# Kernel optimization log

Hardware: AMD Instinct MI355X
Metric: run time of the kernel (lower is better)

## Reference

```python
import jax, jax.numpy as jnp
import numpy as np

SIZE = 128
WIN = SIZE // 4   # sliding-window size == region size (32)
HALF = WIN // 2   # 16


def _conv(x, w, pad, groups=1):
    return jax.lax.conv_general_dilated(x, w, (1, 1), [(pad, pad), (pad, pad)],
        dimension_numbers=('NCHW', 'OIHW', 'NCHW'), feature_group_count=groups)


def _resize(x, h, w):
    # F.interpolate(..., mode='bilinear', align_corners=False)
    return jax.image.resize(x, (x.shape[0], x.shape[1], h, w), 'bilinear', antialias=False)


def _gauss_kernels():
    ax = np.linspace(-2.0, 2.0, 5)
    xx, yy = np.meshgrid(ax, ax)
    g = np.exp(-(xx ** 2 + yy ** 2) / 2.0) / (2.0 * np.pi)  # sigma = 1
    gx = (-xx * g).astype(np.float32)
    gy = (-yy * g).astype(np.float32)
    return (jnp.asarray(np.tile(gx[None, None], (3, 3, 1, 1))),
            jnp.asarray(np.tile(gy[None, None], (3, 3, 1, 1))))


def _edge_extract(x):
    Gx, Gy = _gauss_kernels()
    h = _conv(x, Gx, 2)
    v = _conv(x, Gy, 2)
    return jnp.tanh(jnp.sqrt(h * h + v * v + 1e-8))


def _color_moments(x, win=5):
    # F.unfold-based local mean / unbiased var / skewness, via depthwise box sums
    C = x.shape[1]
    n = float(win * win)
    ones = jnp.ones((C, 1, win, win), x.dtype)
    box = lambda z: _conv(z, ones, win // 2, groups=C)
    s1 = box(x); s2 = box(x * x); s3 = box(x * x * x)
    mean = s1 / n
    var = (s2 - n * mean * mean) / (n - 1.0)               # unbiased, matches torch.var
    m3 = (s3 - 3.0 * mean * s2 + 2.0 * n * mean ** 3) / n  # E[(x-m)^3]
    skew = m3 / (jnp.sqrt(jnp.maximum(var, 0.0)) ** 3 + 1e-6)
    return jnp.concatenate([mean, var, skew], 1)


def _locate_region(c):
    # scipy: gradient magnitude < 0.2 -> 4-connected label at argmax -> bbox center
    H, W = c.shape
    flat = jnp.argmax(c)
    xm = (flat // W).astype(jnp.int32)
    ym = (flat % W).astype(jnp.int32)
    gm = jnp.hypot(jnp.gradient(c, axis=0), jnp.gradient(c, axis=1))
    mask = gm < 0.2
    seed = jnp.zeros((H, W), bool).at[xm, ym].set(True) & mask

    def dil(r):
        d = r
        d = d | jnp.pad(r[1:, :], ((0, 1), (0, 0)))
        d = d | jnp.pad(r[:-1, :], ((1, 0), (0, 0)))
        d = d | jnp.pad(r[:, 1:], ((0, 0), (0, 1)))
        d = d | jnp.pad(r[:, :-1], ((0, 0), (1, 0)))
        return d & mask

    def body(s):
        r, _ = s
        nr = dil(r)
        return (nr, jnp.any(nr != r))

    region, _ = jax.lax.while_loop(lambda s: s[1], body, (seed, jnp.any(seed)))
    rows = jnp.any(region, 1); cols = jnp.any(region, 0)
    rs = jnp.argmax(rows); re = H - jnp.argmax(rows[::-1])
    cs = jnp.argmax(cols); ce = W - jnp.argmax(cols[::-1])
    ok = mask[xm, ym]  # label_at_max != 0
    x1 = jnp.where(ok, ((rs + re) // 2).astype(jnp.int32), xm)
    y1 = jnp.where(ok, ((cs + ce) // 2).astype(jnp.int32), ym)
    return x1, y1


def _affine_grid(move, H, W):
    # theta = [[1,0,tx],[0,1,ty]] with (tx,ty)=move, align_corners=False
    bx = (2.0 * jnp.arange(W, dtype=jnp.float32) + 1.0) / W - 1.0
    by = (2.0 * jnp.arange(H, dtype=jnp.float32) + 1.0) / H - 1.0
    gx = bx[None, None, :] + move[:, 0, None, None]
    gy = by[None, :, None] + move[:, 1, None, None]
    return jnp.stack(jnp.broadcast_arrays(gx, gy), -1)  # [B,H,W,2]


def _grid_sample(x, grid):
    # bilinear, zeros padding, align_corners=False (torch defaults)
    B, C, H, W = x.shape
    ix = ((grid[..., 0] + 1.0) * W - 1.0) / 2.0
    iy = ((grid[..., 1] + 1.0) * H - 1.0) / 2.0
    ix0 = jnp.floor(ix).astype(jnp.int32)
    iy0 = jnp.floor(iy).astype(jnp.int32)
    wx1 = ix - ix0; wy1 = iy - iy0
    b = jnp.arange(B)[:, None, None]

    def g(yy, xx):
        valid = ((xx >= 0) & (xx < W) & (yy >= 0) & (yy < H)).astype(x.dtype)
        v = x[b, :, jnp.clip(yy, 0, H - 1), jnp.clip(xx, 0, W - 1)]  # [B,Hg,Wg,C]
        return v * valid[..., None]

    out = (g(iy0, ix0) * ((1 - wy1) * (1 - wx1))[..., None]
         + g(iy0, ix0 + 1) * ((1 - wy1) * wx1)[..., None]
         + g(iy0 + 1, ix0) * (wy1 * (1 - wx1))[..., None]
         + g(iy0 + 1, ix0 + 1) * (wy1 * wx1)[..., None])
    return jnp.transpose(out, (0, 3, 1, 2))


def _bn_relu6(x, w, b):
    # BatchNorm2d in training mode (batch stats, biased var, eps=1e-5) + ReLU6
    m = x.mean((0, 2, 3), keepdims=True)
    v = ((x - m) ** 2).mean((0, 2, 3), keepdims=True)
    y = (x - m) / jnp.sqrt(v + 1e-5) * w[None, :, None, None] + b[None, :, None, None]
    return jnp.clip(y, 0.0, 6.0)


def setup_inputs():
    key = jax.random.key(0)
    ks = jax.random.split(key, 8)
    B, C = 8, 64
    return dict(
        warm_flag=1,
        feat1=jax.random.normal(ks[0], (B, C, SIZE, SIZE), jnp.float32),
        feat2=jax.random.normal(ks[1], (B, C, SIZE, SIZE), jnp.float32),
        cam1=jax.random.uniform(ks[2], (B, 64, 64), jnp.float32),
        cam2=jax.random.uniform(ks[3], (B, 64, 64), jnp.float32),
        f_g=jax.random.uniform(ks[4], (B, 3, 512, 512), jnp.float32),
        f_e=jax.random.uniform(ks[5], (B, 3, 512, 512), jnp.float32),
        conv1_w=jax.random.normal(ks[6], (C, 3, 3, 3), jnp.float32) * 0.1,
        conv1_b=jnp.zeros((C,), jnp.float32),
        conv2_w=jax.random.normal(ks[7], (C, 9, 3, 3), jnp.float32) * 0.1,
        conv2_b=jnp.zeros((C,), jnp.float32),
        bn_w=jnp.ones((C,), jnp.float32),
        bn_b=jnp.zeros((C,), jnp.float32),
    )


def reference(warm_flag, feat1, feat2, cam1, cam2, f_g, f_e,
              conv1_w, conv1_b, conv2_w, conv2_b, bn_w, bn_b):
    B = cam1.shape[0]
    c1 = _resize(cam1[:, None], SIZE, SIZE)
    c2 = _resize(cam2[:, None], SIZE, SIZE)

    if warm_flag == 1:
        # numpy/scipy path in torch is detached from autograd
        c1s = jax.lax.stop_gradient(c1)
        c2s = jax.lax.stop_gradient(c2)
        x1, y1 = jax.vmap(_locate_region)(c1s[:, 0])
        # valid-mode box convolution of cam2 with ones((H//4, W//4)), argmax
        box = jax.lax.conv_general_dilated(c2s, jnp.ones((1, 1, WIN, WIN), c2.dtype), (1, 1),
            'VALID', dimension_numbers=('NCHW', 'OIHW', 'NCHW'))[:, 0]
        Wv = box.shape[-1]
        flat = jnp.argmax(box.reshape(B, -1), -1)
        x2 = (flat // Wv + HALF).astype(jnp.int32)
        y2 = (flat % Wv + HALF).astype(jnp.int32)

        idx = jnp.arange(SIZE)
        def rect(xc, yc):
            r = (idx[None, :] >= jnp.maximum(xc - HALF, 0)[:, None]) & \
                (idx[None, :] < jnp.minimum(xc + HALF, SIZE)[:, None])
            cc = (idx[None, :] >= jnp.maximum(yc - HALF, 0)[:, None]) & \
                 (idx[None, :] < jnp.minimum(yc + HALF, SIZE)[:, None])
            return r[:, None, :, None] & cc[:, None, None, :]
        mask1 = rect(x1, y1).astype(feat1.dtype)
        mask2 = rect(x2, y2).astype(feat2.dtype)
        mi1 = jnp.stack([x1, y1], -1).astype(jnp.float32)
        mi2 = jnp.stack([x2, y2], -1).astype(jnp.float32)
    else:
        mask1 = jnp.zeros_like(feat1)
        mask2 = jnp.zeros_like(feat2)
        mi1 = jnp.zeros((B, 2), jnp.float32)
        mi2 = jnp.zeros((B, 2), jnp.float32)

    cam2_move = (mi2 - mi1) / (SIZE // 2)
    cam1_move = (mi1 - mi2) / (SIZE // 2)
    grid1 = _affine_grid(cam1_move, SIZE, SIZE)
    grid2 = _affine_grid(cam2_move, SIZE, SIZE)

    moments = _resize(_color_moments(f_e), SIZE, SIZE)   # [B,9,128,128]
    edge = _resize(_edge_extract(f_g), SIZE, SIZE)       # [B,3,128,128]
    feat1_edge = jnp.clip(_conv(edge, conv1_w, 1) + conv1_b[None, :, None, None], 0.0, 6.0)
    feat2_color = _conv(moments, conv2_w, 1) + conv2_b[None, :, None, None]

    feat2_move = _grid_sample(feat2_color * mask2, grid2)
    feat1_edge_move = _grid_sample(feat1_edge * mask1, grid1)

    Bc, C, H, W = feat1.shape
    f1 = feat1.reshape(Bc, C, -1)
    f2 = feat2.reshape(Bc, C, -1)
    f2m = feat2_move.reshape(Bc, C, -1)
    f1m = feat1_edge_move.reshape(Bc, C, -1)

    f2_attn = jax.nn.softmax(jnp.einsum('bcn,bdn->bcd', f2m, f1), -1)  # [B,C,C]
    feat1_apply = jnp.einsum('bcd,bdn->bcn', f2_attn, f1).reshape(Bc, C, H, W)
    f1_attn = jax.nn.softmax(jnp.einsum('bcn,bdn->bcd', f1m, f2), -1)
    feat2_apply = jnp.einsum('bcd,bdn->bcn', f1_attn, f2).reshape(Bc, C, H, W)

    feat1_apply = _bn_relu6(feat1_apply, bn_w, bn_b)
    feat2_apply = _bn_relu6(feat2_apply, bn_w, bn_b)

    if warm_flag == 0:
        return (feat1, feat2, grid1, grid2, feat1_edge, feat2_color, f1_attn, f2_attn, feat1, feat2)
    return (feat1_apply, feat2_apply, grid1, grid2, feat1_edge, feat2_color, f1_attn, f2_attn, feat1, feat2)
```

## Files before the change

kernel.cpp:

```cpp
#include <hip/hip_runtime.h>
#include <math.h>

#define SIZE 128
#define WIN 32
#define HALF 16
#define B 8
#define C 64
#define N (SIZE*SIZE)
#define BCN 8388608
#define BV 97

#define O_APPLY1   0
#define O_APPLY2   8388608
#define O_GRID1    16777216
#define O_GRID2    17039360
#define O_EDGEF    17301504
#define O_COLORF   25690112
#define O_ATTN1    34078720
#define O_ATTN2    34111488
#define O_FEAT1    34144256
#define O_FEAT2    42532864

#define WS_BNP     0
#define WS_XY      361472
#define WS_MOM     361600
#define WS_EDGE    1541248
#define WS_BN      1737856

#define NEGINF (-3.402823466e+38f)

typedef unsigned __int128 u128;

__device__ __forceinline__ u128 hfill(u128 g, u128 m) {
  u128 p = m;
  g |= p & (g << 1);  p &= p << 1;
  g |= p & (g << 2);  p &= p << 2;
  g |= p & (g << 4);  p &= p << 4;
  g |= p & (g << 8);  p &= p << 8;
  g |= p & (g << 16); p &= p << 16;
  g |= p & (g << 32); p &= p << 32;
  g |= p & (g << 64);
  p = m;
  g |= p & (g >> 1);  p &= p >> 1;
  g |= p & (g >> 2);  p &= p >> 2;
  g |= p & (g >> 4);  p &= p >> 4;
  g |= p & (g >> 8);  p &= p >> 8;
  g |= p & (g >> 16); p &= p >> 16;
  g |= p & (g >> 32); p &= p >> 32;
  g |= p & (g >> 64);
  return g;
}

__device__ __forceinline__ float resamp(const float* raw, int i, int j) {
  float fy = fminf(fmaxf(0.5f * (float)i - 0.25f, 0.f), 63.f);
  float fx = fminf(fmaxf(0.5f * (float)j - 0.25f, 0.f), 63.f);
  int y0 = (int)fy; float ty = fy - (float)y0; int y1i = min(y0 + 1, 63);
  int x0 = (int)fx; float tx = fx - (float)x0; int x1i = min(x0 + 1, 63);
  float a00 = raw[y0 * 64 + x0],  a01 = raw[y0 * 64 + x1i];
  float a10 = raw[y1i * 64 + x0], a11 = raw[y1i * 64 + x1i];
  return (1.f - ty) * ((1.f - tx) * a00 + tx * a01)
       + ty * ((1.f - tx) * a10 + tx * a11);
}

#define FRONT_B   8
#define PREP_BASE 16
#define COPY_BASE 2064
#define COPY_BLKS 1024
#define STAGE1_GRID (COPY_BASE + 2 * COPY_BLKS)

__global__ __launch_bounds__(256, 4) void k_stage1(
    const float* __restrict__ cam1, const float* __restrict__ cam2,
    int* __restrict__ xy,
    const float* __restrict__ fe, const float* __restrict__ fg,
    float* __restrict__ mom, float* __restrict__ edge,
    const float4* __restrict__ f1, float4* __restrict__ o8,
    const float4* __restrict__ f2, float4* __restrict__ o9) {
  __shared__ __align__(16) float smem[5632];
  int blk = blockIdx.x;
  int tid = threadIdx.x;

  if (blk >= COPY_BASE) {
    int c = blk - COPY_BASE;
    const float4* s; float4* d;
    if (c < COPY_BLKS) { s = f1; d = o8; }
    else               { s = f2; d = o9; c -= COPY_BLKS; }
    int base = c * 2048 + tid;
    float4 v0 = s[base];
    float4 v1 = s[base + 256];
    float4 v2 = s[base + 512];
    float4 v3 = s[base + 768];
    float4 v4 = s[base + 1024];
    float4 v5 = s[base + 1280];
    float4 v6 = s[base + 1536];
    float4 v7 = s[base + 1792];
    d[base]        = v0;
    d[base + 256]  = v1;
    d[base + 512]  = v2;
    d[base + 768]  = v3;
    d[base + 1024] = v4;
    d[base + 1280] = v5;
    d[base + 1536] = v6;
    d[base + 1792] = v7;
    return;
  }

  if (blk >= PREP_BASE) {
    float* sx = smem;
    int pblk = blk - PREP_BASE;
    if (pblk < 1536) {
      int tile = pblk & 63, ch = (pblk >> 6) % 3, b = pblk / 192;
      int ti0 = (tile >> 3) * 16, tj0 = (tile & 7) * 16;
      const float* src = fe + (size_t)(b * 3 + ch) * 262144;
      int oy0 = 4 * ti0 - 1, ox0 = 4 * tj0 - 1;
      for (int l = tid; l < 66 * 66; l += 256) {
        int r = l / 66, cc = l % 66;
        int gy = oy0 + r, gx = ox0 + cc;
        sx[l] = (gy >= 0 && gy < 512 && gx >= 0 && gx < 512) ? src[gy * 512 + gx] : 0.f;
      }
      __syncthreads();
      int ii = tid >> 4, jj = tid & 15;
      int i = ti0 + ii, j = tj0 + jj;
      float s1a[6], s2a[6], s3a[6], s1b[6], s2b[6], s3b[6];
      #pragma unroll
      for (int t = 0; t < 6; ++t) {
        float a1 = 0, a2 = 0, a3 = 0, b1 = 0, b2 = 0, b3 = 0;
        int lx = 4 * jj + t;
        #pragma unroll
        for (int r = 0; r < 6; ++r) {
          float v = sx[(4 * ii + r) * 66 + lx];
          float v2 = v * v, v3 = v2 * v;
          if (r < 5) { a1 += v; a2 += v2; a3 += v3; }
          if (r > 0) { b1 += v; b2 += v2; b3 += v3; }
        }
        s1a[t] = a1; s2a[t] = a2; s3a[t] = a3;
        s1b[t] = b1; s2b[t] = b2; s3b[t] = b3;
      }
      float am = 0, av = 0, as = 0;
      #pragma unroll
      for (int py = 0; py < 2; ++py) {
        #pragma unroll
        for (int px = 0; px < 2; ++px) {
          float s1 = 0, s2 = 0, s3 = 0;
          #pragma unroll
          for (int t = 0; t < 5; ++t) {
            s1 += py ? s1b[px + t] : s1a[px + t];
            s2 += py ? s2b[px + t] : s2a[px + t];
            s3 += py ? s3b[px + t] : s3a[px + t];
          }
          float mean = s1 / 25.f;
          float var  = (s2 - 25.f * mean * mean) / 24.f;
          float m3   = (s3 - 3.f * mean * s2 + 50.f * mean * mean * mean) / 25.f;
          float sq   = sqrtf(fmaxf(var, 0.f));
          float skew = m3 / (sq * sq * sq + 1e-6f);
          am += mean; av += var; as += skew;
        }
      }
      int base = (b * 9 + ch) * N + i * 128 + j;
      mom[base]         = 0.25f * am;
      mom[base + 3 * N] = 0.25f * av;
      mom[base + 6 * N] = 0.25f * as;
    } else {
      int eblk = pblk - 1536;
      int tile = eblk & 63, b = eblk >> 6;
      int ti0 = (tile >> 3) * 16, tj0 = (tile & 7) * 16;
      const float* s0 = fg + (size_t)b * 3 * 262144;
      int oy0 = 4 * ti0 - 1, ox0 = 4 * tj0 - 1;
      for (int l = tid; l < 66 * 66; l += 256) {
        int r = l / 66, cc = l % 66;
        int gy = oy0 + r, gx = ox0 + cc;
        float v = 0.f;
        if (gy >= 0 && gy < 512 && gx >= 0 && gx < 512) {
          int o = gy * 512 + gx;
          v = s0[o] + s0[262144 + o] + s0[524288 + o];
        }
        sx[l] = v;
      }
      __syncthreads();
      int ii = tid >> 4, jj = tid & 15;
      int i = ti0 + ii, j = tj0 + jj;
      const float INV2PI = 0.15915494309189535f;
      float wg[5], ug[5];
      #pragma unroll
      for (int t = 0; t < 5; ++t) {
        float a = (float)t - 2.f;
        float e = expf(-0.5f * a * a);
        wg[t] = e; ug[t] = -a * e;
      }
      float rAa[6], rAb[6], rBa[6], rBb[6];
      #pragma unroll
      for (int t = 0; t < 6; ++t) {
        float aa = 0, ab = 0, ba = 0, bb = 0;
        int lx = 4 * jj + t;
        #pragma unroll
        for (int r = 0; r < 6; ++r) {
          float v = sx[(4 * ii + r) * 66 + lx];
          if (r < 5) { aa += v * wg[r]; ba += v * ug[r]; }
          if (r > 0) { ab += v * wg[r - 1]; bb += v * ug[r - 1]; }
        }
        rAa[t] = aa; rAb[t] = ab; rBa[t] = ba; rBb[t] = bb;
      }
      float acc = 0.f;
      #pragma unroll
      for (int py = 0; py < 2; ++py) {
        #pragma unroll
        for (int px = 0; px < 2; ++px) {
          float h = 0, v = 0;
          #pragma unroll
          for (int t = 0; t < 5; ++t) {
            float A  = py ? rAb[px + t] : rAa[px + t];
            float Bw = py ? rBb[px + t] : rBa[px + t];
            h += A * ug[t];
            v += Bw * wg[t];
          }
          h *= INV2PI; v *= INV2PI;
          acc += tanhf(sqrtf(h * h + v * v + 1e-8f));
        }
      }
      edge[b * N + i * 128 + j] = 0.25f * acc;
    }
    return;
  }

  if (blk >= FRONT_B) {
    int b = blk - FRONT_B;
    float* raw = smem;
    float* buf = smem + 4096;
    float* sv  = smem + 5120;
    int*   si  = (int*)(smem + 5376);

    const float4* c4 = (const float4*)(cam2 + b * 4096);
    float4* r4 = (float4*)raw;
    #pragma unroll
    for (int k = 0; k < 4; ++k) r4[k * 256 + tid] = c4[k * 256 + tid];
    __syncthreads();

    float bv = NEGINF; int bi = 0;
    for (int r0 = 0; r0 < BV; r0 += 8) {
      int nr = min(8, BV - r0);
      for (int idx = tid; idx < nr * 128; idx += 256) {
        int rr = r0 + (idx >> 7), cc = idx & 127;
        float acc = 0.f;
        for (int dy = 0; dy < WIN; ++dy) acc += resamp(raw, rr + dy, cc);
        buf[idx] = acc;
      }
      __syncthreads();
      for (int q = tid; q < nr * BV; q += 256) {
        int rr = q / BV, cc = q % BV;
        float s = 0.f;
        #pragma unroll
        for (int dx = 0; dx < WIN; ++dx) s += buf[rr * 128 + cc + dx];
        if (s > bv) { bv = s; bi = (r0 + rr) * BV + cc; }
      }
      __syncthreads();
    }
    sv[tid] = bv; si[tid] = bi;
    __syncthreads();
    for (int s = 128; s; s >>= 1) {
      if (tid < s) {
        float ov = sv[tid + s]; int oi = si[tid + s];
        if (ov > sv[tid] || (ov == sv[tid] && oi < si[tid])) { sv[tid] = ov; si[tid] = oi; }
      }
      __syncthreads();
    }
    if (tid == 0) {
      xy[16 + b] = si[0] / BV + HALF;
      xy[24 + b] = si[0] % BV + HALF;
    }
    return;
  }

  {
    int b = blk;
    float* raw = smem;
    float* sv  = smem + 4096;
    int*   si  = (int*)(smem + 4352);
    unsigned long long* mask64 = (unsigned long long*)(smem + 4608);
    int* sint = (int*)(smem + 5120);

    const float4* c4 = (const float4*)(cam1 + b * 4096);
    float4* r4 = (float4*)raw;
    #pragma unroll
    for (int k = 0; k < 4; ++k) r4[k * 256 + tid] = c4[k * 256 + tid];
    __syncthreads();

    float bv = NEGINF; int bi = 0;
    for (int k = 0; k < 64; ++k) {
      int pix = k * 256 + tid;
      float v1 = resamp(raw, pix >> 7, pix & 127);
      if (v1 > bv) { bv = v1; bi = pix; }
    }
    sv[tid] = bv; si[tid] = bi;
    __syncthreads();
    for (int s = 128; s; s >>= 1) {
      if (tid < s) {
        float ov = sv[tid + s]; int oi = si[tid + s];
        if (ov > sv[tid] || (ov == sv[tid] && oi < si[tid])) { sv[tid] = ov; si[tid] = oi; }
      }
      __syncthreads();
    }
    if (tid == 0) { sint[0] = si[0] >> 7; sint[1] = si[0] & 127; }
    __syncthreads();
    int s_xm = sint[0], s_ym = sint[1];

    for (int k = 0; k < 64; ++k) {
      int pix = k * 256 + tid;
      int i = pix >> 7, j = pix & 127;
      float gx_, gy_;
      if (i == 0)        gx_ = resamp(raw, 1, j) - resamp(raw, 0, j);
      else if (i == 127) gx_ = resamp(raw, 127, j) - resamp(raw, 126, j);
      else               gx_ = 0.5f * (resamp(raw, i + 1, j) - resamp(raw, i - 1, j));
      if (j == 0)        gy_ = resamp(raw, i, 1) - resamp(raw, i, 0);
      else if (j == 127) gy_ = resamp(raw, i, 127) - resamp(raw, i, 126);
      else               gy_ = 0.5f * (resamp(raw, i, j + 1) - resamp(raw, i, j - 1));
      bool pred = hypotf(gx_, gy_) < 0.2f;
      unsigned long long bal = __ballot(pred);
      if ((tid & 63) == 0) mask64[(i << 1) + (j >> 6)] = bal;
    }
    __syncthreads();
    if (tid == 0) {
      unsigned long long wdd = mask64[(s_xm << 1) + (s_ym >> 6)];
      sint[2] = (int)((wdd >> (s_ym & 63)) & 1ull);
    }
    __syncthreads();
    int s_ok = sint[2];

    if (tid < 64) {
      int l = tid;
      u128 m0 = ((u128)mask64[4 * l])     | ((u128)mask64[4 * l + 1] << 64);
      u128 m1 = ((u128)mask64[4 * l + 2]) | ((u128)mask64[4 * l + 3] << 64);
      u128 g0 = 0, g1v = 0;
      if (s_ok && (s_xm >> 1) == l) {
        if ((s_xm & 1) == 0) g0  = ((u128)1) << s_ym;
        else                 g1v = ((u128)1) << s_ym;
      }
      g0  = hfill(g0 & m0, m0);
      g1v = hfill(g1v & m1, m1);
      for (;;) {
        unsigned long long ulo = __shfl_up((unsigned long long)g1v, 1);
        unsigned long long uhi = __shfl_up((unsigned long long)(g1v >> 64), 1);
        u128 up = (l > 0) ? (((u128)ulo) | ((u128)uhi << 64)) : (u128)0;
        unsigned long long dlo = __shfl_down((unsigned long long)g0, 1);
        unsigned long long dhi = __shfl_down((unsigned long long)(g0 >> 64), 1);
        u128 dn = (l < 63) ? (((u128)dlo) | ((u128)dhi << 64)) : (u128)0;
        u128 n0 = hfill((g0 | up | g1v) & m0, m0);
        u128 n1 = hfill((g1v | n0 | dn) & m1, m1);
        bool chg = (n0 != g0) || (n1 != g1v);
        g0 = n0; g1v = n1;
        if (!__any(chg)) break;
      }
      unsigned long long be = __ballot(g0 != 0);
      unsigned long long bo = __ballot(g1v != 0);
      unsigned long long cl = (unsigned long long)(g0 | g1v);
      unsigned long long chh = (unsigned long long)((g0 | g1v) >> 64);
      for (int off = 32; off; off >>= 1) {
        cl  |= __shfl_xor(cl, off);
        chh |= __shfl_xor(chh, off);
      }
      if (l == 0) {
        int rs = 0, re = 0, cs_ = 0, ce = 0;
        if (be | bo) {
          int af = be ? (__ffsll(be) - 1) : 1000;
          int bf = bo ? (__ffsll(bo) - 1) : 1000;
          rs = min(af * 2, bf * 2 + 1);
          int al = be ? (63 - __clzll(be)) : -1000;
          int bl = bo ? (63 - __clzll(bo)) : -1000;
          re = max(al * 2, bl * 2 + 1) + 1;
          cs_ = cl ? (__ffsll(cl) - 1) : 64 + (__ffsll(chh) - 1);
          ce = chh ? 128 - __clzll(chh) : 64 - __clzll(cl);
        }
        int x1, y1;
        if (s_ok) { x1 = (rs + re) >> 1; y1 = (cs_ + ce) >> 1; }
        else      { x1 = s_xm;           y1 = s_ym; }
        xy[b] = x1; xy[8 + b] = y1;
      }
    }
  }
}

__global__ __launch_bounds__(256) void k_conv12(
    const float* __restrict__ edge, const float* __restrict__ w1,
    const float* __restrict__ b1, float* __restrict__ o4,
    const float* __restrict__ mom, const float* __restrict__ w2,
    const float* __restrict__ b2, float* __restrict__ o5,
    const int* __restrict__ xy, float* __restrict__ g1, float* __restrict__ g2) {
  __shared__ float tin[9 * 324];
  __shared__ float wsm[64 * 84];
  int tid = threadIdx.x;

  if (blockIdx.x >= 512) {
    if (blockIdx.y != 0) return;
    int b = blockIdx.x - 512;
    float x1f = (float)xy[b], y1f = (float)xy[8 + b];
    float x2f = (float)xy[16 + b], y2f = (float)xy[24 + b];
    float m1x = (x1f - x2f) / 64.f, m1y = (y1f - y2f) / 64.f;
    float* g1b = g1 + (size_t)b * N * 2;
    float* g2b = g2 + (size_t)b * N * 2;
    for (int k = 0; k < 64; ++k) {
      int pix = k * 256 + tid;
      int h = pix >> 7, w = pix & 127;
      float bx = (2.f * (float)w + 1.f) / 128.f - 1.f;
      float by = (2.f * (float)h + 1.f) / 128.f - 1.f;
      g1b[pix * 2]     = bx + m1x; g1b[pix * 2 + 1] = by + m1y;
      g2b[pix * 2]     = bx - m1x; g2b[pix * 2 + 1] = by - m1y;
    }
    return;
  }

  int b = blockIdx.x >> 6, tile = blockIdx.x & 63;
  int ti0 = (tile >> 3) * 16, tj0 = (tile & 7) * 16;
  int i = tid >> 4, j = tid & 15;
  if (blockIdx.y == 0) {
    for (int l = tid; l < 324; l += 256) {
      int r = l / 18, cc = l % 18;
      int gi = ti0 + r - 1, gj = tj0 + cc - 1;
      tin[l] = (gi >= 0 && gi < 128 && gj >= 0 && gj < 128) ? edge[b * N + gi * 128 + gj] : 0.f;
    }
    for (int l = tid; l < 64 * 12; l += 256) {
      int o = l / 12, t = l % 12;
      wsm[l] = (t < 9) ? (w1[o * 27 + t] + w1[o * 27 + 9 + t] + w1[o * 27 + 18 + t]) : 0.f;
    }
    __syncthreads();
    float win[12];
    #pragma unroll
    for (int dy = 0; dy < 3; ++dy)
      #pragma unroll
      for (int dx = 0; dx < 3; ++dx)
        win[dy * 3 + dx] = tin[(i + dy) * 18 + (j + dx)];
    win[9] = 0.f; win[10] = 0.f; win[11] = 0.f;
    float* o = o4 + (size_t)b * C * N + (ti0 + i) * 128 + tj0 + j;
    for (int oc = 0; oc < C; ++oc) {
      const float4* wr = (const float4*)(wsm + oc * 12);
      float acc = b1[oc];
      #pragma unroll
      for (int q = 0; q < 3; ++q) {
        float4 w4 = wr[q];
        acc += w4.x * win[4 * q] + w4.y * win[4 * q + 1]
             + w4.z * win[4 * q + 2] + w4.w * win[4 * q + 3];
      }
      o[oc * N] = fminf(fmaxf(acc, 0.f), 6.f);
    }
  } else {
    for (int l = tid; l < 9 * 324; l += 256) {
      int ic = l / 324, rem = l % 324, r = rem / 18, cc = rem % 18;
      int gi = ti0 + r - 1, gj = tj0 + cc - 1;
      tin[l] = (gi >= 0 && gi < 128 && gj >= 0 && gj < 128) ? mom[(b * 9 + ic) * N + gi * 128 + gj] : 0.f;
    }
    for (int l = tid; l < 64 * 84; l += 256) {
      int o = l / 84, t = l % 84;
      wsm[l] = (t < 81) ? w2[o * 81 + t] : 0.f;
    }
    __syncthreads();
    float win[84];
    #pragma unroll
    for (int ic = 0; ic < 9; ++ic)
      #pragma unroll
      for (int dy = 0; dy < 3; ++dy)
        #pragma unroll
        for (int dx = 0; dx < 3; ++dx)
          win[ic * 9 + dy * 3 + dx] = tin[ic * 324 + (i + dy) * 18 + (j + dx)];
    win[81] = 0.f; win[82] = 0.f; win[83] = 0.f;
    float* o = o5 + (size_t)b * C * N + (ti0 + i) * 128 + tj0 + j;
    for (int oc = 0; oc < C; ++oc) {
      const float4* wr = (const float4*)(wsm + oc * 84);
      float acc = b2[oc];
      #pragma unroll
      for (int q = 0; q < 21; ++q) {
        float4 w4 = wr[q];
        acc += w4.x * win[4 * q] + w4.y * win[4 * q + 1]
             + w4.z * win[4 * q + 2] + w4.w * win[4 * q + 3];
      }
      o[oc * N] = acc;
    }
  }
}

__global__ __launch_bounds__(256) void k_logits(const float* __restrict__ aB1,
                                                const float* __restrict__ bB1,
                                                const float* __restrict__ aB2,
                                                const float* __restrict__ bB2,
                                                float* __restrict__ lg,
                                                const int* __restrict__ xy) {
  int mode = blockIdx.y;
  const float* aBase = mode ? aB2 : aB1;
  const float* bBase = mode ? bB2 : bB1;
  int b = blockIdx.x >> 4, sl = blockIdx.x & 15;
  int tid = threadIdx.x;
  int ci = (tid >> 4) << 2, di = (tid & 15) << 2;
  float* o = lg + (size_t)(((mode * 8 + b) * 16 + sl)) * 4096;

  int x1 = xy[b], y1 = xy[8 + b], x2 = xy[16 + b], y2 = xy[24 + b];
  int dyh, dxw, rlo, rhi, clo, chi;
  if (mode == 0) {
    dyh = y1 - y2; dxw = x1 - x2;
    rlo = max(x1 - HALF, 0); rhi = min(x1 + HALF, SIZE);
    clo = max(y1 - HALF, 0); chi = min(y1 + HALF, SIZE);
  } else {
    dyh = y2 - y1; dxw = x2 - x1;
    rlo = max(x2 - HALF, 0); rhi = min(x2 + HALF, SIZE);
    clo = max(y2 - HALF, 0); chi = min(y2 + HALF, SIZE);
  }
  int hlo = max(0, rlo - dyh), hhi = min(SIZE, rhi - dyh);
  int wlo = max(0, clo - dxw), whi = min(SIZE, chi - dxw);
  int wn = whi - wlo, hn = hhi - hlo;
  int npos = (wn > 0 && hn > 0) ? wn * hn : 0;
  if (sl * 64 >= npos) {
    #pragma unroll
    for (int u = 0; u < 4; ++u)
      #pragma unroll
      for (int v = 0; v < 4; ++v)
        o[(ci + u) * 64 + (di + v)] = 0.f;
    return;
  }

  __shared__ float aS[64][65];
  __shared__ float bS[64][65];
  const float* aB = aBase + (size_t)b * C * N;
  const float* bB = bBase + (size_t)b * C * N;
  for (int l = tid; l < 4096; l += 256) {
    int ch = l >> 6, k = l & 63;
    int p = sl * 64 + k;
    float av = 0.f, bv = 0.f;
    if (p < npos) {
      int h = hlo + p / wn, w = wlo + p % wn;
      av = aB[ch * N + (h + dyh) * 128 + (w + dxw)];
      bv = bB[ch * N + h * 128 + w];
    }
    aS[ch][k] = av; bS[ch][k] = bv;
  }
  __syncthreads();
  float acc[4][4] = {};
  #pragma unroll 4
  for (int k = 0; k < 64; ++k) {
    float a0 = aS[ci][k], a1 = aS[ci + 1][k], a2 = aS[ci + 2][k], a3 = aS[ci + 3][k];
    float b0 = bS[di][k], b1v = bS[di + 1][k], b2v = bS[di + 2][k], b3 = bS[di + 3][k];
    acc[0][0] += a0 * b0; acc[0][1] += a0 * b1v; acc[0][2] += a0 * b2v; acc[0][3] += a0 * b3;
    acc[1][0] += a1 * b0; acc[1][1] += a1 * b1v; acc[1][2] += a1 * b2v; acc[1][3] += a1 * b3;
    acc[2][0] += a2 * b0; acc[2][1] += a2 * b1v; acc[2][2] += a2 * b2v; acc[2][3] += a2 * b3;
    acc[3][0] += a3 * b0; acc[3][1] += a3 * b1v; acc[3][2] += a3 * b2v; acc[3][3] += a3 * b3;
  }
  #pragma unroll
  for (int u = 0; u < 4; ++u)
    #pragma unroll
    for (int v = 0; v < 4; ++v)
      o[(ci + u) * 64 + (di + v)] = acc[u][v];
}

__global__ void k_softmax(const float* __restrict__ lg,
                          float* __restrict__ o6, float* __restrict__ o7) {
  int row = blockIdx.x;
  int mode = blockIdx.y;
  float* dst = mode ? o7 : o6;
  int b = row >> 6, c = row & 63;
  int lane = threadIdx.x;
  const float* base = lg + (size_t)((mode * 8 + b) * 16) * 4096 + c * 64 + lane;
  float v = 0.f;
  #pragma unroll
  for (int sl = 0; sl < 16; ++sl) v += base[sl * 4096];
  float mx = v;
  for (int off = 32; off; off >>= 1) mx = fmaxf(mx, __shfl_xor(mx, off));
  float e = expf(v - mx);
  float s = e;
  for (int off = 32; off; off >>= 1) s += __shfl_xor(s, off);
  dst[row * 64 + lane] = e / s;
}

__global__ __launch_bounds__(256) void k_applyst(const float* __restrict__ a1,
                                                 const float* __restrict__ s1_,
                                                 float* __restrict__ d1,
                                                 const float* __restrict__ a2,
                                                 const float* __restrict__ s2_,
                                                 float* __restrict__ d2,
                                                 float* __restrict__ bnp) {
  const float* attn; const float* src; float* dst;
  int t = blockIdx.y;
  if (t == 0) { attn = a1; src = s1_; dst = d1; }
  else        { attn = a2; src = s2_; dst = d2; }
  int b = blockIdx.x >> 6, chunk = blockIdx.x & 63;
  int n0 = chunk * 256 + threadIdx.x;
  const float* s = src + (size_t)b * C * N + n0;
  float v[64];
  #pragma unroll
  for (int d = 0; d < 64; ++d) v[d] = s[d * N];
  const float4* at4 = (const float4*)(attn + b * 4096);
  float* o = dst + (size_t)b * C * N + n0;
  __shared__ float red[64][4], red2[64][4];
  int lane = threadIdx.x & 63, wave = threadIdx.x >> 6;
  for (int c = 0; c < 64; ++c) {
    float acc = 0.f;
    #pragma unroll
    for (int q = 0; q < 16; ++q) {
      float4 w4 = at4[c * 16 + q];
      acc += w4.x * v[4 * q] + w4.y * v[4 * q + 1] + w4.z * v[4 * q + 2] + w4.w * v[4 * q + 3];
    }
    o[c * N] = acc;
    float sr = acc, ssr = acc * acc;
    for (int off = 32; off; off >>= 1) {
      sr  += __shfl_xor(sr, off);
      ssr += __shfl_xor(ssr, off);
    }
    if (lane == 0) { red[c][wave] = sr; red2[c][wave] = ssr; }
  }
  __syncthreads();
  if (threadIdx.x < 64) {
    int c = threadIdx.x;
    float sr  = red[c][0] + red[c][1] + red[c][2] + red[c][3];
    float ssr = red2[c][0] + red2[c][1] + red2[c][2] + red2[c][3];
    int idx = (t * 64 + c) * 512 + blockIdx.x;
    bnp[idx]         = sr;
    bnp[65536 + idx] = ssr;
  }
}

__global__ void k_bnstats2(const float* __restrict__ bnp, float* __restrict__ stats) {
  __shared__ float sr[128][4], ssr[128][4];
  int tid = threadIdx.x;
  int combo = tid >> 2, q = tid & 3;
  float s = 0.f, ss = 0.f;
  for (int k = 0; k < 128; ++k) {
    int idx = combo * 512 + q * 128 + k;
    s  += bnp[idx];
    ss += bnp[65536 + idx];
  }
  sr[combo][q] = s; ssr[combo][q] = ss;
  __syncthreads();
  if (q == 0) {
    float S  = sr[combo][0] + sr[combo][1] + sr[combo][2] + sr[combo][3];
    float SS = ssr[combo][0] + ssr[combo][1] + ssr[combo][2] + ssr[combo][3];
    int t = combo >> 6, c = combo & 63;
    float mean = S / 131072.f;
    float var  = SS / 131072.f - mean * mean;
    stats[t * 128 + c]      = mean;
    stats[t * 128 + 64 + c] = 1.f / sqrtf(var + 1e-5f);
  }
}

__global__ __launch_bounds__(256) void k_bnapply(
    float4* __restrict__ o0, float4* __restrict__ o1,
    const float* __restrict__ stats,
    const float* __restrict__ bw, const float* __restrict__ bb) {
  int i = blockIdx.x * 256 + threadIdx.x;
  int t = blockIdx.y;
  float4* p = t ? o1 : o0;
  int c = (i >> 12) & 63;
  float m = stats[t * 128 + c], r = stats[t * 128 + 64 + c];
  float w_ = bw[c], b_ = bb[c];
  float4 v = p[i];
  v.x = fminf(fmaxf((v.x - m) * r * w_ + b_, 0.f), 6.f);
  v.y = fminf(fmaxf((v.y - m) * r * w_ + b_, 0.f), 6.f);
  v.z = fminf(fmaxf((v.z - m) * r * w_ + b_, 0.f), 6.f);
  v.w = fminf(fmaxf((v.w - m) * r * w_ + b_, 0.f), 6.f);
  p[i] = v;
}

extern "C" void kernel_launch(void* const* d_in, const int* in_sizes, int n_in,
                              void* d_out, int out_size, void* d_ws, size_t ws_size,
                              hipStream_t stream) {
  const float* feat1   = (const float*)d_in[1];
  const float* feat2   = (const float*)d_in[2];
  const float* cam1    = (const float*)d_in[3];
  const float* cam2    = (const float*)d_in[4];
  const float* f_g     = (const float*)d_in[5];
  const float* f_e     = (const float*)d_in[6];
  const float* conv1_w = (const float*)d_in[7];
  const float* conv1_b = (const float*)d_in[8];
  const float* conv2_w = (const float*)d_in[9];
  const float* conv2_b = (const float*)d_in[10];
  const float* bn_w    = (const float*)d_in[11];
  const float* bn_b    = (const float*)d_in[12];

  float* out = (float*)d_out;
  float* w = (float*)d_ws;
  int* xy = (int*)(w + WS_XY);

  float* o0 = out + O_APPLY1;
  float* o1 = out + O_APPLY2;
  float* o2 = out + O_GRID1;
  float* o3 = out + O_GRID2;
  float* o4 = out + O_EDGEF;
  float* o5 = out + O_COLORF;
  float* o6 = out + O_ATTN1;
  float* o7 = out + O_ATTN2;
  float* o8 = out + O_FEAT1;
  float* o9 = out + O_FEAT2;

  k_stage1<<<STAGE1_GRID, 256, 0, stream>>>(
      cam1, cam2, xy,
      f_e, f_g, w + WS_MOM, w + WS_EDGE,
      (const float4*)feat1, (float4*)o8, (const float4*)feat2, (float4*)o9);

  k_conv12<<<dim3(520, 2), 256, 0, stream>>>(w + WS_EDGE, conv1_w, conv1_b, o4,
                                             w + WS_MOM, conv2_w, conv2_b, o5,
                                             xy, o2, o3);

  k_logits<<<dim3(B * 16, 2), 256, 0, stream>>>(o4, feat2, o5, feat1,
                                                w + WS_MOM, xy);

  k_softmax<<<dim3(B * C, 2), 64, 0, stream>>>(w + WS_MOM, o6, o7);

  k_applyst<<<dim3(B * 64, 2), 256, 0, stream>>>(o7, feat1, o0, o6, feat2, o1,
                                                 w + WS_BNP);

  k_bnstats2<<<1, 512, 0, stream>>>(w + WS_BNP, w + WS_BN);

  k_bnapply<<<dim3(BCN / 4 / 256, 2), 256, 0, stream>>>(
      (float4*)o0, (float4*)o1, w + WS_BN, bn_w, bn_b);
}
```

Measured before the change: 536.0 us.

## Split cam2 window-argmax across row chunks and precompute resampled rows

The cam2 sliding-window argmax was done by one block per batch, looping over all 97 row offsets and recomputing the bilinear resample 32 times per column sum. It now launches 13 chunk blocks per batch. Each block resamples its needed rows into shared memory once, computes column sums from them, and writes a partial max/index to workspace. The final reduction across chunks happens in the grid-building blocks of k_conv12, which also write xy. The aim is to shorten the serial critical path of stage1. The cost is more shared memory (lower occupancy bound from 4 to 3) and reuse of the BN-partials workspace region for the partials.

```diff
diff --git a/kernel.cpp b/kernel.cpp
--- a/kernel.cpp
+++ b/kernel.cpp
@@ -62,20 +62,22 @@
        + ty * ((1.f - tx) * a10 + tx * a11);
 }
 
-#define FRONT_B   8
-#define PREP_BASE 16
-#define COPY_BASE 2064
-#define COPY_BLKS 1024
+#define FRONT_B     8
+#define NCHUNK      13
+#define PREP_BASE   112
+#define COPY_BASE   2160
+#define COPY_BLKS   1024
 #define STAGE1_GRID (COPY_BASE + 2 * COPY_BLKS)
 
-__global__ __launch_bounds__(256, 4) void k_stage1(
+__global__ __launch_bounds__(256, 3) void k_stage1(
     const float* __restrict__ cam1, const float* __restrict__ cam2,
     int* __restrict__ xy,
     const float* __restrict__ fe, const float* __restrict__ fg,
     float* __restrict__ mom, float* __restrict__ edge,
     const float4* __restrict__ f1, float4* __restrict__ o8,
-    const float4* __restrict__ f2, float4* __restrict__ o9) {
-  __shared__ __align__(16) float smem[5632];
+    const float4* __restrict__ f2, float4* __restrict__ o9,
+    float* __restrict__ pval, int* __restrict__ pidx) {
+  __shared__ __align__(16) float smem[10752];
   int blk = blockIdx.x;
   int tid = threadIdx.x;
 
@@ -222,11 +224,17 @@
   }
 
   if (blk >= FRONT_B) {
-    int b = blk - FRONT_B;
-    float* raw = smem;
-    float* buf = smem + 4096;
-    float* sv  = smem + 5120;
-    int*   si  = (int*)(smem + 5376);
+    int cid = blk - FRONT_B;
+    int b = cid / NCHUNK, chunk = cid % NCHUNK;
+    int r0 = chunk * 8;
+    int nr = min(8, BV - r0);
+    int nrows = nr + WIN - 1;
+
+    float* raw  = smem;
+    float* rows = smem + 4096;
+    float* csum = smem + 9216;
+    float* sv   = smem + 10240;
+    int*   si   = (int*)(smem + 10496);
 
     const float4* c4 = (const float4*)(cam2 + b * 4096);
     float4* r4 = (float4*)raw;
@@ -234,24 +242,29 @@
     for (int k = 0; k < 4; ++k) r4[k * 256 + tid] = c4[k * 256 + tid];
     __syncthreads();
 
+    for (int l = tid; l < nrows * 128; l += 256) {
+      int q = l >> 7, c = l & 127;
+      rows[l] = resamp(raw, r0 + q, c);
+    }
+    __syncthreads();
+
+    for (int l = tid; l < nr * 128; l += 256) {
+      int q = l >> 7, c = l & 127;
+      float acc = 0.f;
+      #pragma unroll
+      for (int dy = 0; dy < WIN; ++dy) acc += rows[(q + dy) * 128 + c];
+      csum[l] = acc;
+    }
+    __syncthreads();
+
     float bv = NEGINF; int bi = 0;
-    for (int r0 = 0; r0 < BV; r0 += 8) {
-      int nr = min(8, BV - r0);
-      for (int idx = tid; idx < nr * 128; idx += 256) {
-        int rr = r0 + (idx >> 7), cc = idx & 127;
-        float acc = 0.f;
-        for (int dy = 0; dy < WIN; ++dy) acc += resamp(raw, rr + dy, cc);
-        buf[idx] = acc;
-      }
-      __syncthreads();
-      for (int q = tid; q < nr * BV; q += 256) {
-        int rr = q / BV, cc = q % BV;
-        float s = 0.f;
-        #pragma unroll
-        for (int dx = 0; dx < WIN; ++dx) s += buf[rr * 128 + cc + dx];
-        if (s > bv) { bv = s; bi = (r0 + rr) * BV + cc; }
-      }
-      __syncthreads();
+    for (int p = tid; p < nr * BV; p += 256) {
+      int q = p / BV, cc = p % BV;
+      float s = 0.f;
+      #pragma unroll
+      for (int dx = 0; dx < WIN; ++dx) s += csum[q * 128 + cc + dx];
+      int gidx = (r0 + q) * BV + cc;
+      if (s > bv || (s == bv && gidx < bi)) { bv = s; bi = gidx; }
     }
     sv[tid] = bv; si[tid] = bi;
     __syncthreads();
@@ -262,10 +275,7 @@
       }
       __syncthreads();
     }
-    if (tid == 0) {
-      xy[16 + b] = si[0] / BV + HALF;
-      xy[24 + b] = si[0] % BV + HALF;
-    }
+    if (tid == 0) { pval[b * NCHUNK + chunk] = sv[0]; pidx[b * NCHUNK + chunk] = si[0]; }
     return;
   }
 
@@ -382,7 +392,8 @@
     const float* __restrict__ b1, float* __restrict__ o4,
     const float* __restrict__ mom, const float* __restrict__ w2,
     const float* __restrict__ b2, float* __restrict__ o5,
-    const int* __restrict__ xy, float* __restrict__ g1, float* __restrict__ g2) {
+    int* __restrict__ xy, float* __restrict__ g1, float* __restrict__ g2,
+    const float* __restrict__ pval, const int* __restrict__ pidx) {
   __shared__ float tin[9 * 324];
   __shared__ float wsm[64 * 84];
   int tid = threadIdx.x;
@@ -390,8 +401,15 @@
   if (blockIdx.x >= 512) {
     if (blockIdx.y != 0) return;
     int b = blockIdx.x - 512;
+    float bv = NEGINF; int bi = 0;
+    for (int k = 0; k < NCHUNK; ++k) {
+      float v = pval[b * NCHUNK + k]; int ix = pidx[b * NCHUNK + k];
+      if (v > bv || (v == bv && ix < bi)) { bv = v; bi = ix; }
+    }
+    int x2i = bi / BV + HALF, y2i = bi % BV + HALF;
+    if (tid == 0) { xy[16 + b] = x2i; xy[24 + b] = y2i; }
     float x1f = (float)xy[b], y1f = (float)xy[8 + b];
-    float x2f = (float)xy[16 + b], y2f = (float)xy[24 + b];
+    float x2f = (float)x2i, y2f = (float)y2i;
     float m1x = (x1f - x2f) / 64.f, m1y = (y1f - y2f) / 64.f;
     float* g1b = g1 + (size_t)b * N * 2;
     float* g2b = g2 + (size_t)b * N * 2;
@@ -671,6 +689,8 @@
   float* out = (float*)d_out;
   float* w = (float*)d_ws;
   int* xy = (int*)(w + WS_XY);
+  float* pval = w + WS_BNP;
+  int*   pidx = (int*)(w + WS_BNP + 128);
 
   float* o0 = out + O_APPLY1;
   float* o1 = out + O_APPLY2;
@@ -686,11 +706,12 @@
   k_stage1<<<STAGE1_GRID, 256, 0, stream>>>(
       cam1, cam2, xy,
       f_e, f_g, w + WS_MOM, w + WS_EDGE,
-      (const float4*)feat1, (float4*)o8, (const float4*)feat2, (float4*)o9);
+      (const float4*)feat1, (float4*)o8, (const float4*)feat2, (float4*)o9,
+      pval, pidx);
 
   k_conv12<<<dim3(520, 2), 256, 0, stream>>>(w + WS_EDGE, conv1_w, conv1_b, o4,
                                              w + WS_MOM, conv2_w, conv2_b, o5,
-                                             xy, o2, o3);
+                                             xy, o2, o3, pval, pidx);
 
   k_logits<<<dim3(B * 16, 2), 256, 0, stream>>>(o4, feat2, o5, feat1,
                                                 w + WS_MOM, xy);
```

After: 536.3 us. About the same (+0.1%).
